# Kernel optimization log

Measured on AMD Instinct MI355X. Metric: run time of the kernel, lower is better.

The kernel has to match this reference:

```python
import jax, jax.numpy as jnp
import numpy as np

NEG_BIG = -1e12
ALPHA = 0.2  # LeakyReLU negative slope

def setup_inputs() -> dict:
    key = jax.random.key(0)
    k1, k2, k3, k4, k5 = jax.random.split(key, 5)
    N, F_in, F_out = 8192, 256, 128
    inp = jax.random.normal(k1, (N, F_in), dtype=jnp.float32)
    adj = jax.random.randint(k2, (N, N), 0, 2, dtype=jnp.int32)
    W = jax.random.normal(k3, (F_in, F_out), dtype=jnp.float32) * 0.05
    W_2 = jax.random.normal(k4, (F_in, F_out), dtype=jnp.float32) * 0.05
    W_3 = jax.random.normal(k5, (F_in, F_out), dtype=jnp.float32) * 0.05
    return {"inp": inp, "adj": adj, "W": W, "W_2": W_2, "W_3": W_3}

def reference(inp, adj, W, W_2, W_3):
    # h = inp @ W, h_2 = inp @ W_2  -> scores e = LeakyReLU(h @ h_2^T)  [N, N]
    h = inp @ W
    h_2 = inp @ W_2
    e = jax.nn.leaky_relu(h @ h_2.T, negative_slope=ALPHA)
    # adjacency mask, row softmax (dropout disabled: eval mode)
    attention = jax.nn.softmax(jnp.where(adj > 0, e, NEG_BIG), axis=1)
    h_3 = inp @ W_3
    h_prime = attention @ h_3
    return jax.nn.elu(h_prime)  # concat=True path
```

## Files before the change

kernel.cpp:

```cpp
#include <hip/hip_runtime.h>
#include <hip/hip_fp16.h>

#define N    8192
#define FIN  256
#define FOUT 128
#define BN   64

typedef _Float16 half8 __attribute__((ext_vector_type(8)));
typedef _Float16 half4v __attribute__((ext_vector_type(4)));
typedef float floatx4 __attribute__((ext_vector_type(4)));

__device__ __forceinline__ float exp2_fast(float x) { return __builtin_amdgcn_exp2f(x); }

__device__ __forceinline__ void gload_lds16(const void* g, void* l) {
    __builtin_amdgcn_global_load_lds(
        (const __attribute__((address_space(1))) void*)g,
        (__attribute__((address_space(3))) void*)l, 16, 0, 0);
}

__global__ __launch_bounds__(256)
void wprep_kernel(const float* __restrict__ W0,
                  const float* __restrict__ W1,
                  const float* __restrict__ W2,
                  _Float16* __restrict__ Wf)
{
    int idx  = blockIdx.x * 256 + threadIdx.x;
    int lane = idx & 63;
    int frag = idx >> 6;
    int w    = frag >> 6;
    int f    = frag & 63;
    int nt   = f >> 3, kc = f & 7;
    int quad = lane >> 4, lo16 = lane & 15;
    const float* Wp = w == 0 ? W0 : (w == 1 ? W1 : W2);
    half8 v;
#pragma unroll
    for (int jj = 0; jj < 8; jj++)
        v[jj] = (_Float16)Wp[(size_t)(kc * 32 + quad * 8 + jj) * FOUT + nt * 16 + lo16];
    *(half8*)&Wf[(size_t)idx * 8] = v;
}

__global__ __launch_bounds__(256, 2)
void gemm3_kernel(const float* __restrict__ inp,
                  const _Float16* __restrict__ Wf,
                  _Float16* __restrict__ H,
                  _Float16* __restrict__ H2,
                  _Float16* __restrict__ H3T)
{
    const int which = blockIdx.z;
    const int c0    = blockIdx.y * 64;
    const _Float16* Wfw = Wf + (size_t)which * 64 * 64 * 8;
    const int r0 = blockIdx.x * 64;
    const int tid  = threadIdx.x;
    const int wave = tid >> 6;
    const int lane = tid & 63;
    const int lo16 = lane & 15;
    const int quad = lane >> 4;
    const int r = r0 + wave * 16 + lo16;

    half8 a[8];
#pragma unroll
    for (int kc = 0; kc < 8; kc++) {
        const float* p = &inp[(size_t)r * FIN + kc * 32 + quad * 8];
        float4 v0 = *(const float4*)p;
        float4 v1 = *(const float4*)(p + 4);
        a[kc][0] = (_Float16)v0.x; a[kc][1] = (_Float16)v0.y;
        a[kc][2] = (_Float16)v0.z; a[kc][3] = (_Float16)v0.w;
        a[kc][4] = (_Float16)v1.x; a[kc][5] = (_Float16)v1.y;
        a[kc][6] = (_Float16)v1.z; a[kc][7] = (_Float16)v1.w;
    }

    floatx4 acc[4];
#pragma unroll
    for (int i = 0; i < 4; i++) acc[i] = (floatx4){0.f, 0.f, 0.f, 0.f};

#pragma unroll
    for (int kc = 0; kc < 8; kc++)
#pragma unroll
        for (int nt = 0; nt < 4; nt++) {
            int ntg = (c0 >> 4) + nt;
            half8 b = *(const half8*)&Wfw[(((size_t)ntg * 8 + kc) * 64 + lane) * 8];
            acc[nt] = __builtin_amdgcn_mfma_f32_16x16x32_f16(a[kc], b, acc[nt], 0, 0, 0);
        }

    const int arow = wave * 16 + quad * 4;
    if (which < 2) {
        _Float16* outp = which == 0 ? H : H2;
        const float scale = which == 0 ? 1.44269504f : 1.0f;
#pragma unroll
        for (int nt = 0; nt < 4; nt++)
#pragma unroll
            for (int rr = 0; rr < 4; rr++)
                outp[(size_t)(r0 + arow + rr) * FOUT + c0 + nt * 16 + lo16] =
                    (_Float16)(acc[nt][rr] * scale);
    } else {
#pragma unroll
        for (int nt = 0; nt < 4; nt++) {
            half4v v;
#pragma unroll
            for (int rr = 0; rr < 4; rr++) v[rr] = (_Float16)acc[nt][rr];
            *(half4v*)&H3T[(size_t)(c0 + nt * 16 + lo16) * N + r0 + arow] = v;
        }
    }
}

__global__ __launch_bounds__(256)
void repackKV_kernel(const _Float16* __restrict__ H2,
                     const _Float16* __restrict__ H3T,
                     _Float16* __restrict__ Kf,
                     _Float16* __restrict__ Vf)
{
    if (blockIdx.x < 512) {
        int idx  = blockIdx.x * 256 + threadIdx.x;
        int lane = idx & 63;
        int frag = idx >> 6;
        int jb = frag >> 4, f = frag & 15;
        int c = f >> 3, ntj = (f >> 2) & 1, kc = f & 3;
        int quad = lane >> 4, lo16 = lane & 15;
        int srcrow = jb * 64 + c * 32 + (lo16 >> 2) * 8 + ntj * 4 + (lo16 & 3);
        half8 v = *(const half8*)&H2[(size_t)srcrow * FOUT + kc * 32 + quad * 8];
        *(half8*)&Kf[(size_t)idx * 8] = v;
    } else {
        int idx  = (blockIdx.x - 512) * 256 + threadIdx.x;
        int lane = idx & 63;
        int frag = idx >> 6;
        int jb = frag >> 4, f = frag & 15, nt = f >> 1, kc = f & 1;
        int quad = lane >> 4, lo16 = lane & 15;
        half8 v = *(const half8*)&H3T[(size_t)(nt * 16 + lo16) * N + jb * 64 + kc * 32 + quad * 8];
        *(half8*)&Vf[(size_t)idx * 8] = v;
    }
}

template<int JS>
__global__ __launch_bounds__(512, 2)
void attn_kernel(const _Float16* __restrict__ Hq,
                 const _Float16* __restrict__ Kf,
                 const _Float16* __restrict__ Vf,
                 const int* __restrict__ adj,
                 float* __restrict__ OpartT,
                 float* __restrict__ mpart,
                 float* __restrict__ lpart)
{
    __shared__ __align__(16) _Float16 KV[2][16384];

    const int tid  = threadIdx.x;
    const int wave = tid >> 6;
    const int lane = tid & 63;
    const int lo16 = lane & 15;
    const int quad = lane >> 4;
    const int qsh  = quad * 2;
    const int bid  = blockIdx.x;
    const int js   = bid & (JS - 1);
    const int ib   = bid / JS;
    const int iw   = ib * 128 + wave * 16;
    const int irow = iw + lo16;
    const int jbeg = js * (N / JS);
    constexpr int NIT = 16;
    const int jb0  = jbeg >> 6;

    half8 q[4];
#pragma unroll
    for (int kc = 0; kc < 4; kc++)
        q[kc] = *(const half8*)&Hq[(size_t)irow * FOUT + kc * 32 + quad * 8];

    floatx4 O[8];
#pragma unroll
    for (int nt = 0; nt < 8; nt++) O[nt] = (floatx4){0.f, 0.f, 0.f, 0.f};
    float m_s = -1e12f, l_s = 0.f;

    const int* arow_base = adj + (size_t)iw * N + jbeg + lane * 4;

    unsigned long long mA[4], mB[4];

    auto STAGE = [&](int nxt, int jbn) {
        const _Float16* gk = Kf + (size_t)jbn * 8192;
        const _Float16* gv = Vf + (size_t)jbn * 8192;
#pragma unroll
        for (int r = 0; r < 2; r++) {
            int goff = (r * 512 + tid) * 8;
            int loff = (r * 512 + wave * 64) * 8;
            gload_lds16(gk + goff, &KV[nxt][loff]);
            gload_lds16(gv + goff, &KV[nxt][8192 + loff]);
        }
    };

    auto BALLOT4 = [&](unsigned long long (&mn)[4], int p,
                       const int4& a0, const int4& a1, const int4& a2, const int4& a3) {
#pragma unroll
        for (int qq = 0; qq < 4; qq++) {
            const int4& a = (qq == 0) ? a0 : (qq == 1) ? a1 : (qq == 2) ? a2 : a3;
            unsigned long long b0 = __ballot(a.x != 0);
            unsigned long long b1 = __ballot(a.y != 0);
            unsigned long long b2 = __ballot(a.z != 0);
            unsigned long long b3 = __ballot(a.w != 0);
            bool sel = (lo16 == p * 4 + qq);
            mn[0] = sel ? b0 : mn[0];
            mn[1] = sel ? b1 : mn[1];
            mn[2] = sel ? b2 : mn[2];
            mn[3] = sel ? b3 : mn[3];
        }
    };

    STAGE(0, jb0);
#pragma unroll
    for (int p = 0; p < 4; p++) {
        const int* rb = arow_base;
        int4 a0 = *(const int4*)(rb + (size_t)(p * 4 + 0) * N);
        int4 a1 = *(const int4*)(rb + (size_t)(p * 4 + 1) * N);
        int4 a2 = *(const int4*)(rb + (size_t)(p * 4 + 2) * N);
        int4 a3 = *(const int4*)(rb + (size_t)(p * 4 + 3) * N);
        BALLOT4(mA, p, a0, a1, a2, a3);
    }
    __syncthreads();

    auto ITER = [&](int it, int p, unsigned long long (&mc)[4],
                    unsigned long long (&mn)[4], bool buildNext, int gnext) {
        const int cur = it & 1;

        int4 a0, a1, a2, a3;
        if (buildNext) {
            const int* rb = arow_base + gnext * 256;
            a0 = *(const int4*)(rb + (size_t)(p * 4 + 0) * N);
            a1 = *(const int4*)(rb + (size_t)(p * 4 + 1) * N);
            a2 = *(const int4*)(rb + (size_t)(p * 4 + 2) * N);
            a3 = *(const int4*)(rb + (size_t)(p * 4 + 3) * N);
        }
        if (it + 1 < NIT) STAGE(cur ^ 1, jb0 + it + 1);

        const _Float16* kb = &KV[cur][0];
        const _Float16* vb = &KV[cur][8192];

        floatx4 S[2][2];
#pragma unroll
        for (int c = 0; c < 2; c++)
#pragma unroll
            for (int ntj = 0; ntj < 2; ntj++) {
                S[c][ntj] = (floatx4){0.f, 0.f, 0.f, 0.f};
#pragma unroll
                for (int kc = 0; kc < 4; kc++) {
                    half8 kf = *(const half8*)&kb[(((c * 2 + ntj) * 4 + kc) * 64 + lane) * 8];
                    S[c][ntj] = __builtin_amdgcn_mfma_f32_16x16x32_f16(kf, q[kc], S[c][ntj], 0, 0, 0);
                }
            }

        float mx = -1e12f;
#pragma unroll
        for (int c = 0; c < 2; c++)
#pragma unroll
            for (int ntj = 0; ntj < 2; ntj++)
#pragma unroll
                for (int r = 0; r < 4; r++) {
                    float e = S[c][ntj][r];
                    e = fmaxf(e, 0.2f * e);
                    S[c][ntj][r] = e;
                    mx = fmaxf(mx, e);
                }
        mx = fmaxf(mx, __shfl_xor(mx, 16));
        mx = fmaxf(mx, __shfl_xor(mx, 32));
        if (__any(mx > m_s + 5.75f)) {
            float mn2 = fmaxf(m_s, mx);
            float al = exp2_fast(m_s - mn2);
            m_s = mn2;
            l_s *= al;
#pragma unroll
            for (int nt = 0; nt < 8; nt++)
#pragma unroll
                for (int r = 0; r < 4; r++)
                    O[nt][r] *= al;
        }

        half8 pb[2];
        float sum = 0.f;
#pragma unroll
        for (int c = 0; c < 2; c++)
#pragma unroll
            for (int ntj = 0; ntj < 2; ntj++)
#pragma unroll
                for (int r = 0; r < 4; r++) {
                    float e = S[c][ntj][r] - m_s;
                    bool bit = (mc[r] >> (p * 16 + c * 8 + ntj + qsh)) & 1ull;
                    float pp = bit ? exp2_fast(e) : 0.f;
                    sum += pp;
                    pb[c][ntj * 4 + r] = (_Float16)pp;
                }
        sum += __shfl_xor(sum, 16);
        sum += __shfl_xor(sum, 32);
        l_s += sum;

#pragma unroll
        for (int c = 0; c < 2; c++)
#pragma unroll
            for (int nt = 0; nt < 8; nt++) {
                half8 vf = *(const half8*)&vb[((nt * 2 + c) * 64 + lane) * 8];
                O[nt] = __builtin_amdgcn_mfma_f32_16x16x32_f16(vf, pb[c], O[nt], 0, 0, 0);
            }

        if (buildNext) BALLOT4(mn, p, a0, a1, a2, a3);

        __syncthreads();
    };

#pragma unroll
    for (int g = 0; g < 4; g++) {
#pragma unroll
        for (int p = 0; p < 4; p++) {
            int it = g * 4 + p;
            if (g & 1) ITER(it, p, mB, mA, g < 3, g + 1);
            else       ITER(it, p, mA, mB, g < 3, g + 1);
        }
    }

#pragma unroll
    for (int nt = 0; nt < 8; nt++)
#pragma unroll
        for (int r = 0; r < 4; r++) {
            int f = nt * 16 + quad * 4 + r;
            OpartT[((size_t)js * FOUT + f) * N + irow] = O[nt][r];
        }
    if (quad == 0) {
        mpart[js * N + irow] = m_s;
        lpart[js * N + irow] = l_s;
    }
}

template<int JS>
__global__ __launch_bounds__(256)
void combine_kernel(const float* __restrict__ OpartT,
                    const float* __restrict__ mpart,
                    const float* __restrict__ lpart,
                    float* __restrict__ out)
{
    int idx = blockIdx.x * 256 + threadIdx.x;
    int f  = idx >> 11;
    int i4 = (idx & 2047) << 2;

    float4 M = {-3e38f, -3e38f, -3e38f, -3e38f};
    float4 m[JS];
#pragma unroll
    for (int s = 0; s < JS; s++) {
        m[s] = *(const float4*)&mpart[s * N + i4];
        M.x = fmaxf(M.x, m[s].x); M.y = fmaxf(M.y, m[s].y);
        M.z = fmaxf(M.z, m[s].z); M.w = fmaxf(M.w, m[s].w);
    }
    float4 L = {0.f, 0.f, 0.f, 0.f};
    float4 o = {0.f, 0.f, 0.f, 0.f};
#pragma unroll
    for (int s = 0; s < JS; s++) {
        float4 l = *(const float4*)&lpart[s * N + i4];
        float4 w;
        w.x = exp2_fast(m[s].x - M.x); w.y = exp2_fast(m[s].y - M.y);
        w.z = exp2_fast(m[s].z - M.z); w.w = exp2_fast(m[s].w - M.w);
        L.x += l.x * w.x; L.y += l.y * w.y;
        L.z += l.z * w.z; L.w += l.w * w.w;
        float4 v = *(const float4*)&OpartT[((size_t)s * FOUT + f) * N + i4];
        o.x += w.x * v.x; o.y += w.y * v.y;
        o.z += w.z * v.z; o.w += w.w * v.w;
    }
    float r0 = o.x / L.x, r1 = o.y / L.y, r2 = o.z / L.z, r3 = o.w / L.w;
    out[(size_t)(i4 + 0) * FOUT + f] = r0 > 0.f ? r0 : __expf(r0) - 1.f;
    out[(size_t)(i4 + 1) * FOUT + f] = r1 > 0.f ? r1 : __expf(r1) - 1.f;
    out[(size_t)(i4 + 2) * FOUT + f] = r2 > 0.f ? r2 : __expf(r2) - 1.f;
    out[(size_t)(i4 + 3) * FOUT + f] = r3 > 0.f ? r3 : __expf(r3) - 1.f;
}

extern "C" void kernel_launch(void* const* d_in, const int* in_sizes, int n_in,
                              void* d_out, int out_size, void* d_ws, size_t ws_size,
                              hipStream_t stream) {
    const float* inp = (const float*)d_in[0];
    const int*   adj = (const int*)d_in[1];
    const float* W0  = (const float*)d_in[2];
    const float* W1  = (const float*)d_in[3];
    const float* W2  = (const float*)d_in[4];
    float* out = (float*)d_out;

    constexpr int JS = 8;
    char* ws = (char*)d_ws;
    _Float16* H    = (_Float16*)(ws);
    _Float16* H2   = (_Float16*)(ws + (2u << 20));
    _Float16* H3T  = (_Float16*)(ws + (4u << 20));
    _Float16* Wf   = (_Float16*)(ws + (6u << 20));
    _Float16* Kf   = (_Float16*)(ws + (7u << 20));
    _Float16* Vf   = (_Float16*)(ws + (9u << 20));
    float* OpartT  = (float*)(ws + (11u << 20));
    float* mpart   = (float*)(ws + (43u << 20));
    float* lpart   = (float*)(ws + (43u << 20) + (size_t)JS * N * sizeof(float));

    wprep_kernel<<<48, 256, 0, stream>>>(W0, W1, W2, Wf);
    gemm3_kernel<<<dim3(N / 64, 2, 3), 256, 0, stream>>>(inp, Wf, H, H2, H3T);
    repackKV_kernel<<<1024, 256, 0, stream>>>(H2, H3T, Kf, Vf);
    attn_kernel<JS><<<(N / 128) * JS, 512, 0, stream>>>(H, Kf, Vf, adj, OpartT, mpart, lpart);
    combine_kernel<JS><<<(FOUT * (N / 4)) / 256, 256, 0, stream>>>(OpartT, mpart, lpart, out);
}
```

Before: 412.9 us.

## Precompute adjacency bitmasks into shared memory before the attention loop

The adjacency ballot masks for the whole j-slice are now built in a prologue and stored in a per-wave shared-memory table. Previously they were built incrementally inside the main loop, one group ahead, using double-buffered registers. The main loop now just reads four 64-bit masks from LDS per iteration. This removes adj global loads and ballots from the MFMA loop and frees mask registers, but it front-loads all adj loads before any compute starts and adds 16 KB of LDS, which may affect occupancy at 2 blocks/CU.

```diff
diff --git a/kernel.cpp b/kernel.cpp
--- a/kernel.cpp
+++ b/kernel.cpp
@@ -141,6 +141,7 @@
                  float* __restrict__ lpart)
 {
     __shared__ __align__(16) _Float16 KV[2][16384];
+    __shared__ unsigned long long ML[8 * 256];
 
     const int tid  = threadIdx.x;
     const int wave = tid >> 6;
@@ -167,10 +168,6 @@
     for (int nt = 0; nt < 8; nt++) O[nt] = (floatx4){0.f, 0.f, 0.f, 0.f};
     float m_s = -1e12f, l_s = 0.f;
 
-    const int* arow_base = adj + (size_t)iw * N + jbeg + lane * 4;
-
-    unsigned long long mA[4], mB[4];
-
     auto STAGE = [&](int nxt, int jbn) {
         const _Float16* gk = Kf + (size_t)jbn * 8192;
         const _Float16* gv = Vf + (size_t)jbn * 8192;
@@ -183,48 +180,45 @@
         }
     };
 
-    auto BALLOT4 = [&](unsigned long long (&mn)[4], int p,
-                       const int4& a0, const int4& a1, const int4& a2, const int4& a3) {
-#pragma unroll
-        for (int qq = 0; qq < 4; qq++) {
-            const int4& a = (qq == 0) ? a0 : (qq == 1) ? a1 : (qq == 2) ? a2 : a3;
-            unsigned long long b0 = __ballot(a.x != 0);
-            unsigned long long b1 = __ballot(a.y != 0);
-            unsigned long long b2 = __ballot(a.z != 0);
-            unsigned long long b3 = __ballot(a.w != 0);
-            bool sel = (lo16 == p * 4 + qq);
-            mn[0] = sel ? b0 : mn[0];
-            mn[1] = sel ? b1 : mn[1];
-            mn[2] = sel ? b2 : mn[2];
-            mn[3] = sel ? b3 : mn[3];
-        }
-    };
-
     STAGE(0, jb0);
-#pragma unroll
-    for (int p = 0; p < 4; p++) {
-        const int* rb = arow_base;
-        int4 a0 = *(const int4*)(rb + (size_t)(p * 4 + 0) * N);
-        int4 a1 = *(const int4*)(rb + (size_t)(p * 4 + 1) * N);
-        int4 a2 = *(const int4*)(rb + (size_t)(p * 4 + 2) * N);
-        int4 a3 = *(const int4*)(rb + (size_t)(p * 4 + 3) * N);
-        BALLOT4(mA, p, a0, a1, a2, a3);
+
+    unsigned long long* MLb = &ML[wave * 256];
+    {
+        const int* ab = adj + (size_t)iw * N + jbeg + lane * 4;
+#pragma unroll
+        for (int b = 0; b < 8; b++) {
+            int4 av[8];
+#pragma unroll
+            for (int x = 0; x < 8; x++) {
+                int r16 = b * 2 + (x >> 2);
+                int g   = x & 3;
+                av[x] = *(const int4*)(ab + (size_t)r16 * N + g * 256);
+            }
+#pragma unroll
+            for (int x = 0; x < 8; x++) {
+                int r16 = b * 2 + (x >> 2);
+                int g   = x & 3;
+                unsigned long long b0 = __ballot(av[x].x != 0);
+                unsigned long long b1 = __ballot(av[x].y != 0);
+                unsigned long long b2 = __ballot(av[x].z != 0);
+                unsigned long long b3 = __ballot(av[x].w != 0);
+                unsigned long long v = lane == 0 ? b0 : (lane == 1 ? b1 : (lane == 2 ? b2 : b3));
+                if (lane < 4) MLb[(g * 4 + lane) * 16 + r16] = v;
+            }
+        }
     }
     __syncthreads();
 
-    auto ITER = [&](int it, int p, unsigned long long (&mc)[4],
-                    unsigned long long (&mn)[4], bool buildNext, int gnext) {
+    auto ITER = [&](int it) {
         const int cur = it & 1;
-
-        int4 a0, a1, a2, a3;
-        if (buildNext) {
-            const int* rb = arow_base + gnext * 256;
-            a0 = *(const int4*)(rb + (size_t)(p * 4 + 0) * N);
-            a1 = *(const int4*)(rb + (size_t)(p * 4 + 1) * N);
-            a2 = *(const int4*)(rb + (size_t)(p * 4 + 2) * N);
-            a3 = *(const int4*)(rb + (size_t)(p * 4 + 3) * N);
-        }
+        const int p   = it & 3;
+
         if (it + 1 < NIT) STAGE(cur ^ 1, jb0 + it + 1);
+
+        unsigned long long mc[4];
+#pragma unroll
+        for (int r = 0; r < 4; r++)
+            mc[r] = MLb[((it >> 2) * 4 + r) * 16 + lo16];
 
         const _Float16* kb = &KV[cur][0];
         const _Float16* vb = &KV[cur][8192];
@@ -294,20 +288,12 @@
                 O[nt] = __builtin_amdgcn_mfma_f32_16x16x32_f16(vf, pb[c], O[nt], 0, 0, 0);
             }
 
-        if (buildNext) BALLOT4(mn, p, a0, a1, a2, a3);
-
         __syncthreads();
     };
 
 #pragma unroll
-    for (int g = 0; g < 4; g++) {
-#pragma unroll
-        for (int p = 0; p < 4; p++) {
-            int it = g * 4 + p;
-            if (g & 1) ITER(it, p, mB, mA, g < 3, g + 1);
-            else       ITER(it, p, mA, mB, g < 3, g + 1);
-        }
-    }
+    for (int it = 0; it < NIT; it++)
+        ITER(it);
 
 #pragma unroll
     for (int nt = 0; nt < 8; nt++)
```

After: 446.1 us. 8.0% more time.
